# Optimization experiments

Measured on AMD Instinct MI355X. Metric: run time of the kernel, lower is better.

## Reference

```python
import jax, jax.numpy as jnp
import numpy as np

NUM_CLASSES = 3
POS_T, NEG_T = 0.5, 0.3
RATIO = 3
W_OBJ, W_CLS, W_LOC = 1.0, 1.0, 2.0


def _pairwise_iou(a, b):
    # a: [N,4] anchors, b: [G,4] gt boxes, xyxy
    ix1 = jnp.maximum(a[:, None, 0], b[None, :, 0])
    iy1 = jnp.maximum(a[:, None, 1], b[None, :, 1])
    ix2 = jnp.minimum(a[:, None, 2], b[None, :, 2])
    iy2 = jnp.minimum(a[:, None, 3], b[None, :, 3])
    inter = jnp.clip(ix2 - ix1, 0) * jnp.clip(iy2 - iy1, 0)
    area_a = (a[:, 2] - a[:, 0]) * (a[:, 3] - a[:, 1])
    area_b = (b[:, 2] - b[:, 0]) * (b[:, 3] - b[:, 1])
    union = area_a[:, None] + area_b[None, :] - inter
    return inter / jnp.maximum(union, 1e-9)


def _masked_mean(x, m):
    c = m.sum()
    return jnp.where(c > 0, (x * m).sum() / jnp.maximum(c, 1.0), 0.0)


def _per_image(pred, anc, ax, ay, aw, ah, boxes_gt, labels_gt):
    # pred: [N, 5+nc]; anc: [N,4]; boxes_gt: [G,4]; labels_gt: [G] in 1..nc
    iou = _pairwise_iou(anc, boxes_gt)              # [N, G]
    best = jnp.argmax(iou, axis=1)
    best_iou = jnp.max(iou, axis=1)
    pos = best_iou >= POS_T
    neg = best_iou < NEG_T
    mb = boxes_gt[best]                             # matched boxes [N,4]
    ml = labels_gt[best]                            # matched labels [N]
    obj_logit = pred[:, 4]
    cls_logit = pred[:, 5:]
    obj_t = pos.astype(pred.dtype)
    # BCEWithLogits (numerically stable)
    obj_loss = jnp.maximum(obj_logit, 0) - obj_logit * obj_t + jnp.log1p(jnp.exp(-jnp.abs(obj_logit)))
    # hard negative mining: top-(3*num_pos) detached obj losses among negatives
    num_pos = pos.sum()
    k = jnp.minimum(RATIO * num_pos, neg.sum())
    cand = jnp.where(neg, jax.lax.stop_gradient(obj_loss), -1.0)
    order = jnp.argsort(-cand)
    ranks = jnp.zeros_like(order).at[order].set(jnp.arange(order.shape[0], dtype=order.dtype))
    sel_neg = neg & (ranks < k)
    loss_obj = _masked_mean(obj_loss, (pos | sel_neg).astype(pred.dtype))
    # classification over positives, labels shifted to 0-based
    logp = jax.nn.log_softmax(cls_logit, axis=-1)
    tgt = jnp.clip(ml - 1, 0)
    ce = -jnp.take_along_axis(logp, tgt[:, None], axis=1)[:, 0]
    loss_cls = _masked_mean(ce, pos.astype(pred.dtype))
    # localization over positives: SmoothL1 on encoded offsets
    gx = (mb[:, 0] + mb[:, 2]) * 0.5
    gy = (mb[:, 1] + mb[:, 3]) * 0.5
    gw = jnp.maximum(mb[:, 2] - mb[:, 0], 1e-6)
    gh = jnp.maximum(mb[:, 3] - mb[:, 1], 1e-6)
    loc_tgt = jnp.stack([(gx - ax) / aw, (gy - ay) / ah,
                         jnp.log(gw / aw), jnp.log(gh / ah)], axis=1)
    d = pred[:, :4] - loc_tgt
    ad = jnp.abs(d)
    sl1 = jnp.where(ad < 1.0, 0.5 * d * d, ad - 0.5)  # [N,4]
    pm = pos.astype(pred.dtype)
    cnt = 4.0 * pm.sum()
    loss_loc = jnp.where(cnt > 0, (sl1 * pm[:, None]).sum() / jnp.maximum(cnt, 1.0), 0.0)
    return loss_obj, loss_cls, loss_loc


def _detection_loss(preds, ancs, gt_boxes, gt_labels):
    B = preds[0].shape[0]
    obj_s = 0.0
    cls_s = 0.0
    loc_s = 0.0
    for pred, anc in zip(preds, ancs):
        Bp, C, H, W = pred.shape
        p = jnp.transpose(pred, (0, 2, 3, 1)).reshape(Bp, -1, 5 + NUM_CLASSES)
        ax = (anc[:, 0] + anc[:, 2]) * 0.5
        ay = (anc[:, 1] + anc[:, 3]) * 0.5
        aw = jnp.maximum(anc[:, 2] - anc[:, 0], 1e-6)
        ah = jnp.maximum(anc[:, 3] - anc[:, 1], 1e-6)
        lo, lc, ll = jax.vmap(
            lambda pb, bb, lb: _per_image(pb, anc, ax, ay, aw, ah, bb, lb)
        )(p, gt_boxes, gt_labels)
        obj_s = obj_s + lo.sum()
        cls_s = cls_s + lc.sum()
        loc_s = loc_s + ll.sum()
    obj_m = obj_s / B
    cls_m = cls_s / B
    loc_m = loc_s / B
    total = W_OBJ * obj_m + W_CLS * cls_m + W_LOC * loc_m
    return total, obj_m, cls_m, loc_m


def setup_inputs() -> dict:
    key = jax.random.key(0)
    k = jax.random.split(key, 8)
    B, G, A = 32, 50, 3
    img = 512.0
    scales = [(128, 128), (64, 64), (32, 32)]
    C = A * (5 + NUM_CLASSES)  # 24

    def make_anchors(H, W):
        stride = img / H
        ys, xs = np.meshgrid(np.arange(H), np.arange(W), indexing="ij")
        cx = (xs + 0.5) * stride
        cy = (ys + 0.5) * stride
        per = []
        for s in (1.0, 1.5, 2.0):
            half = s * stride
            per.append(np.stack([cx - half, cy - half, cx + half, cy + half], axis=-1).reshape(-1, 4))
        b = np.stack(per, axis=1).reshape(-1, 4)  # [H*W*A, 4], A innermost
        return jnp.asarray(b, dtype=jnp.float32)

    preds = [jax.random.normal(k[i], (B, C, H, W), dtype=jnp.float32) for i, (H, W) in enumerate(scales)]
    ancs = [make_anchors(H, W) for (H, W) in scales]
    cx = jax.random.uniform(k[3], (B, G)) * 384.0 + 64.0
    cy = jax.random.uniform(k[4], (B, G)) * 384.0 + 64.0
    w = jax.random.uniform(k[5], (B, G)) * 112.0 + 16.0
    h = jax.random.uniform(k[6], (B, G)) * 112.0 + 16.0
    gt_boxes = jnp.stack([cx - w / 2, cy - h / 2, cx + w / 2, cy + h / 2], axis=-1).astype(jnp.float32)
    gt_labels = jax.random.randint(k[7], (B, G), 1, NUM_CLASSES + 1)
    return {"p0": preds[0], "p1": preds[1], "p2": preds[2],
            "a0": ancs[0], "a1": ancs[1], "a2": ancs[2],
            "gt_boxes": gt_boxes, "gt_labels": gt_labels}


def reference(p0, p1, p2, a0, a1, a2, gt_boxes, gt_labels):
    return _detection_loss([p0, p1, p2], [a0, a1, a2], gt_boxes, gt_labels)
```

## Files before the change

kernel.cpp:

```cpp
#include <hip/hip_runtime.h>

#define WS_ACC_POS   0
#define WS_ACC_NEG   96
#define WS_ACC_OBJ   192
#define WS_ACC_CLS   288
#define WS_ACC_LOC   384
#define WS_SENT      480
#define WS_H1        512
#define WS_TOTAL_U32 (512 + 96*192*2)

#define NBINS        192
#define BIN_OFF      872
#define SUM_SCALE    33554432.0f
#define INV_SUM_SCALE (1.0f/33554432.0f)

__device__ __forceinline__ float sl1f(float d){
  float ad = fabsf(d); return ad < 1.f ? 0.5f*d*d : ad - 0.5f;
}
__device__ __forceinline__ unsigned int rec_cnt(unsigned int v){
  return (v >= 0xA0000000u) ? (v - 0xAAAAAAAAu) : v;
}

__global__ __launch_bounds__(256) void k_main(
    const float* __restrict__ p0, const float* __restrict__ p1, const float* __restrict__ p2,
    const float* __restrict__ gtb, const int* __restrict__ gtl,
    unsigned int* __restrict__ ws)
{
  const int id = blockIdx.x;
  int s, bIm, chunk, H, lw; const float* p;
  if (id < 2048){ s=0; H=128; lw=7; chunk=id>>5;            bIm=id&31;          p=p0; }
  else if (id < 2560){ s=1; H=64; lw=6; chunk=(id-2048)>>5; bIm=(id-2048)&31;   p=p1; }
  else {              s=2; H=32; lw=5; chunk=(id-2560)>>5;  bIm=(id-2560)&31;   p=p2; }
  const int W = H, HW = H*W;
  const float stride = 512.0f/(float)H;
  const int g = s*32 + bIm;
  const int tid = threadIdx.x;

  __shared__ float4 sBox[52];
  __shared__ float  sArea[52], sGx[52], sGy[52], sGw[52], sGh[52];
  __shared__ int    sLbl[52];
  __shared__ int    sNk;
  __shared__ unsigned long long sH[NBINS];
  __shared__ float  sRF[3][4];
  __shared__ unsigned int sRU[2][4];

  if (tid < 64){
    const int ymin = (chunk*256)>>lw;
    const int rowc = 256>>lw;
    const float by1 = ((float)ymin+0.5f)*stride - 2.0f*stride;
    const float by2 = ((float)(ymin+rowc-1)+0.5f)*stride + 2.0f*stride;
    bool keep=false; float4 gb=make_float4(0,0,0,0); int lbl=0;
    if (tid < 50){
      gb  = *(const float4*)(gtb + ((size_t)bIm*50 + tid)*4);
      lbl = gtl[bIm*50 + tid];
      keep = (fminf(by2, gb.w) - fmaxf(by1, gb.y)) > 0.f;
    }
    unsigned long long m = __ballot(keep);
    if (keep){
      int idx = __popcll(m & ((1ull<<tid)-1ull));
      sBox[idx]=gb;
      sArea[idx]=(gb.z-gb.x)*(gb.w-gb.y);
      sGx[idx]=(gb.x+gb.z)*0.5f;  sGy[idx]=(gb.y+gb.w)*0.5f;
      sGw[idx]=fmaxf(gb.z-gb.x,1e-6f); sGh[idx]=fmaxf(gb.w-gb.y,1e-6f);
      sLbl[idx]=lbl;
    }
    if (tid==0) sNk = __popcll(m);
  }
  if (tid < NBINS) sH[tid]=0ull;
  __syncthreads();

  const int nk = sNk;
  const int hw  = chunk*256 + tid;
  const int hwW = chunk*256 + (tid & ~63);
  const int y = hw>>lw, x = hw&(W-1);
  const float cx = ((float)x+0.5f)*stride, cy = ((float)y+0.5f)*stride;

  const float* pb = p + (size_t)bIm*24*HW + hw;
  float xo[3];
  #pragma unroll
  for (int a=0;a<3;a++) xo[a] = pb[(size_t)(a*8+4)*HW];

  const int wxlo = (W >= 64) ? (hwW & (W-1)) : 0;
  const int wxhi = (W >= 64) ? (wxlo + 63)   : (W-1);
  const int wylo = hwW>>lw, wyhi = (hwW+63)>>lw;
  const float m2 = 2.0f*stride;
  const float wx1 = ((float)wxlo+0.5f)*stride - m2;
  const float wx2 = ((float)wxhi+0.5f)*stride + m2;
  const float wy1 = ((float)wylo+0.5f)*stride - m2;
  const float wy2 = ((float)wyhi+0.5f)*stride + m2;

  float half[3]; half[0]=stride; half[1]=1.5f*stride; half[2]=2.0f*stride;
  float areaA[3], bi[3], bu[3]; int bj[3];
  #pragma unroll
  for (int a=0;a<3;a++){
    const float aw = 2.0f*half[a];
    areaA[a]=aw*aw; bi[a]=0.f; bu[a]=1e-9f; bj[a]=0;
  }
  for (int j=0;j<nk;j++){
    const float4 gb = sBox[j];
    if (gb.x >= wx2 || gb.z <= wx1 || gb.y >= wy2 || gb.w <= wy1) continue;
    const float ar = sArea[j];
    #pragma unroll
    for (int a=0;a<3;a++){
      const float iy1 = fmaxf(cy-half[a], gb.y), iy2 = fminf(cy+half[a], gb.w);
      const float ih  = fmaxf(iy2-iy1, 0.f);
      const float ix1 = fmaxf(cx-half[a], gb.x), ix2 = fminf(cx+half[a], gb.z);
      const float iw  = fmaxf(ix2-ix1, 0.f);
      const float inter = iw*ih;
      const float un = areaA[a] + ar - inter;
      if (inter*bu[a] > bi[a]*un){ bi[a]=inter; bu[a]=un; bj[a]=j; }
    }
  }

  int accPos=0, accNeg=0;
  float accObj=0.f, accCls=0.f, accLoc=0.f;
  #pragma unroll
  for (int a=0;a<3;a++){
    const float bestIou = bi[a]/bu[a];
    const bool pos = bestIou >= 0.5f;
    const bool neg = bestIou < 0.3f;
    if (pos || neg){
      float objl = fmaxf(xo[a],0.f) - (pos ? xo[a] : 0.f)
                 + __logf(1.f + __expf(-fabsf(xo[a])));
      objl = fmaxf(objl, 0.f);
      if (neg){
        accNeg++;
        const int bin = min(max((int)(__float_as_uint(objl)>>20) - BIN_OFF, 0), NBINS-1);
        const unsigned long long pack =
            (1ull<<48) | (unsigned long long)__float2uint_rn(objl * SUM_SCALE);
        atomicAdd(&sH[bin], pack);
      } else {
        accPos++; accObj += objl;
        const int jb = bj[a];
        const float aw = 2.0f*half[a];
        const float c0=pb[(size_t)(a*8+5)*HW], c1=pb[(size_t)(a*8+6)*HW], c2=pb[(size_t)(a*8+7)*HW];
        const float mm = fmaxf(fmaxf(c0,c1),c2);
        const float lse = mm + __logf(__expf(c0-mm)+__expf(c1-mm)+__expf(c2-mm));
        const int t = max(sLbl[jb]-1, 0);
        const float ct = (t==0)?c0 : (t==1)?c1 : c2;
        accCls += lse - ct;
        const float tx = (sGx[jb]-cx)/aw;
        const float ty = (sGy[jb]-cy)/aw;
        const float tw = __logf(sGw[jb]/aw);
        const float th = __logf(sGh[jb]/aw);
        accLoc += sl1f(pb[(size_t)(a*8+0)*HW]-tx) + sl1f(pb[(size_t)(a*8+1)*HW]-ty)
                + sl1f(pb[(size_t)(a*8+2)*HW]-tw) + sl1f(pb[(size_t)(a*8+3)*HW]-th);
      }
    }
  }

  #pragma unroll
  for (int o=32;o;o>>=1){
    accPos += __shfl_down(accPos,o,64);
    accNeg += __shfl_down(accNeg,o,64);
    accObj += __shfl_down(accObj,o,64);
    accCls += __shfl_down(accCls,o,64);
    accLoc += __shfl_down(accLoc,o,64);
  }
  if ((tid & 63)==0){
    const int w = tid>>6;
    sRU[0][w]=(unsigned)accPos; sRU[1][w]=(unsigned)accNeg;
    sRF[0][w]=accObj; sRF[1][w]=accCls; sRF[2][w]=accLoc;
  }
  __syncthreads();
  if (tid==0){
    float* wf = (float*)ws;
    unsigned pc=0, nc=0; float ob=0,cl=0,lc=0;
    #pragma unroll
    for (int w=0;w<4;w++){ pc+=sRU[0][w]; nc+=sRU[1][w]; ob+=sRF[0][w]; cl+=sRF[1][w]; lc+=sRF[2][w]; }
    if (pc) atomicAdd(&ws[WS_ACC_POS+g], pc);
    if (nc) atomicAdd(&ws[WS_ACC_NEG+g], nc);
    if (ob!=0.f) atomicAdd(&wf[WS_ACC_OBJ+g], ob);
    if (cl!=0.f) atomicAdd(&wf[WS_ACC_CLS+g], cl);
    if (lc!=0.f) atomicAdd(&wf[WS_ACC_LOC+g], lc);
  }
  if (tid < NBINS){
    const unsigned long long v = sH[tid];
    if (v){
      unsigned long long* gH = (unsigned long long*)(ws + WS_H1) + (size_t)g*NBINS;
      atomicAdd(&gH[tid], v);
    }
  }
}

__global__ __launch_bounds__(64) void k_select(unsigned int* __restrict__ ws,
                                               float* __restrict__ out){
  const int g = blockIdx.x, lane = threadIdx.x;
  float* wf = (float*)ws;
  __shared__ int   sTie, sR;
  __shared__ float sTieAvg;

  const int pos  = (int)rec_cnt(ws[WS_ACC_POS+g]);
  const int negc = (int)rec_cnt(ws[WS_ACC_NEG+g]);
  const int k = min(3*pos, negc);
  float selSum = 0.f;

  if (k > 0){
    const unsigned long long base =
        (ws[WS_SENT]==0xAAAAAAAAu) ? 0xAAAAAAAAAAAAAAAAull : 0ull;
    const unsigned long long* gH =
        (const unsigned long long*)(ws + WS_H1) + (size_t)g*NBINS;
    unsigned int c[3]; float sm[3];
    #pragma unroll
    for (int j=0;j<3;j++){
      const unsigned long long d = gH[lane*3+j] - base;
      c[j]  = (unsigned int)(d>>48);
      sm[j] = (float)(d & 0xFFFFFFFFFFFFull) * INV_SUM_SCALE;
    }
    const unsigned int c3 = c[0]+c[1]+c[2];
    unsigned int incl = c3;
    #pragma unroll
    for (int off=1; off<64; off<<=1){
      unsigned int yv = __shfl_down(incl, off, 64);
      if (lane+off < 64) incl += yv;
    }
    const unsigned int excl = incl - c3;
    if (lane==0){ sTie = -1; sR = 0; sTieAvg = 0.f; }
    if (excl < (unsigned)k && incl >= (unsigned)k){
      unsigned int cum = excl;
      #pragma unroll
      for (int j=2;j>=0;j--){
        const unsigned int cc = c[j];
        if (cum + cc >= (unsigned)k){
          sTie = lane*3+j; sR = (int)((unsigned)k - cum);
          sTieAvg = sm[j]/(float)cc;
          break;
        }
        cum += cc;
      }
    }
    __syncthreads();
    const int tie = sTie;
    float above = 0.f;
    #pragma unroll
    for (int j=0;j<3;j++) if (lane*3+j > tie) above += sm[j];
    #pragma unroll
    for (int o=32;o;o>>=1) above += __shfl_down(above,o,64);
    selSum = above + (float)sR * sTieAvg;
  }
  if (lane==0){
    const int cObj = pos + k;
    const float lo = (cObj>0) ? (wf[WS_ACC_OBJ+g]+selSum)/(float)cObj : 0.f;
    const float lc = (pos>0)  ? wf[WS_ACC_CLS+g]/(float)pos           : 0.f;
    const float ll = (pos>0)  ? wf[WS_ACC_LOC+g]/(float)(4*pos)       : 0.f;
    const float invB = 1.f/32.f;
    atomicAdd(out+0, (lo + lc + 2.f*ll)*invB);
    atomicAdd(out+1, lo*invB);
    atomicAdd(out+2, lc*invB);
    atomicAdd(out+3, ll*invB);
  }
}

extern "C" void kernel_launch(void* const* d_in, const int* in_sizes, int n_in,
                              void* d_out, int out_size, void* d_ws, size_t ws_size,
                              hipStream_t stream){
  if (ws_size < (size_t)WS_TOTAL_U32*4) return;
  const float* p0  = (const float*)d_in[0];
  const float* p1  = (const float*)d_in[1];
  const float* p2  = (const float*)d_in[2];
  const float* gtb = (const float*)d_in[6];
  const int*   gtl = (const int*)d_in[7];
  unsigned int* ws = (unsigned int*)d_ws;
  float* out = (float*)d_out;

  hipLaunchKernelGGL(k_main,   dim3(2688), dim3(256), 0, stream, p0,p1,p2,gtb,gtl,ws);
  hipLaunchKernelGGL(k_select, dim3(96),   dim3(64),  0, stream, ws, out);
}
```

Measured before the change: 122.4 us.

## Use grid-stride persistent blocks in main kernel and pack pos/neg counters

```diff
diff --git a/kernel.cpp b/kernel.cpp
--- a/kernel.cpp
+++ b/kernel.cpp
@@ -13,6 +13,7 @@
 #define BIN_OFF      872
 #define SUM_SCALE    33554432.0f
 #define INV_SUM_SCALE (1.0f/33554432.0f)
+#define NB_MAIN      896
 
 __device__ __forceinline__ float sl1f(float d){
   float ad = fabsf(d); return ad < 1.f ? 0.5f*d*d : ad - 0.5f;
@@ -26,14 +27,6 @@
     const float* __restrict__ gtb, const int* __restrict__ gtl,
     unsigned int* __restrict__ ws)
 {
-  const int id = blockIdx.x;
-  int s, bIm, chunk, H, lw; const float* p;
-  if (id < 2048){ s=0; H=128; lw=7; chunk=id>>5;            bIm=id&31;          p=p0; }
-  else if (id < 2560){ s=1; H=64; lw=6; chunk=(id-2048)>>5; bIm=(id-2048)&31;   p=p1; }
-  else {              s=2; H=32; lw=5; chunk=(id-2560)>>5;  bIm=(id-2560)&31;   p=p2; }
-  const int W = H, HW = H*W;
-  const float stride = 512.0f/(float)H;
-  const int g = s*32 + bIm;
   const int tid = threadIdx.x;
 
   __shared__ float4 sBox[52];
@@ -42,143 +35,156 @@
   __shared__ int    sNk;
   __shared__ unsigned long long sH[NBINS];
   __shared__ float  sRF[3][4];
-  __shared__ unsigned int sRU[2][4];
-
-  if (tid < 64){
-    const int ymin = (chunk*256)>>lw;
-    const int rowc = 256>>lw;
-    const float by1 = ((float)ymin+0.5f)*stride - 2.0f*stride;
-    const float by2 = ((float)(ymin+rowc-1)+0.5f)*stride + 2.0f*stride;
-    bool keep=false; float4 gb=make_float4(0,0,0,0); int lbl=0;
-    if (tid < 50){
-      gb  = *(const float4*)(gtb + ((size_t)bIm*50 + tid)*4);
-      lbl = gtl[bIm*50 + tid];
-      keep = (fminf(by2, gb.w) - fmaxf(by1, gb.y)) > 0.f;
-    }
-    unsigned long long m = __ballot(keep);
-    if (keep){
-      int idx = __popcll(m & ((1ull<<tid)-1ull));
-      sBox[idx]=gb;
-      sArea[idx]=(gb.z-gb.x)*(gb.w-gb.y);
-      sGx[idx]=(gb.x+gb.z)*0.5f;  sGy[idx]=(gb.y+gb.w)*0.5f;
-      sGw[idx]=fmaxf(gb.z-gb.x,1e-6f); sGh[idx]=fmaxf(gb.w-gb.y,1e-6f);
-      sLbl[idx]=lbl;
-    }
-    if (tid==0) sNk = __popcll(m);
-  }
-  if (tid < NBINS) sH[tid]=0ull;
-  __syncthreads();
-
-  const int nk = sNk;
-  const int hw  = chunk*256 + tid;
-  const int hwW = chunk*256 + (tid & ~63);
-  const int y = hw>>lw, x = hw&(W-1);
-  const float cx = ((float)x+0.5f)*stride, cy = ((float)y+0.5f)*stride;
-
-  const float* pb = p + (size_t)bIm*24*HW + hw;
-  float xo[3];
-  #pragma unroll
-  for (int a=0;a<3;a++) xo[a] = pb[(size_t)(a*8+4)*HW];
-
-  const int wxlo = (W >= 64) ? (hwW & (W-1)) : 0;
-  const int wxhi = (W >= 64) ? (wxlo + 63)   : (W-1);
-  const int wylo = hwW>>lw, wyhi = (hwW+63)>>lw;
-  const float m2 = 2.0f*stride;
-  const float wx1 = ((float)wxlo+0.5f)*stride - m2;
-  const float wx2 = ((float)wxhi+0.5f)*stride + m2;
-  const float wy1 = ((float)wylo+0.5f)*stride - m2;
-  const float wy2 = ((float)wyhi+0.5f)*stride + m2;
-
-  float half[3]; half[0]=stride; half[1]=1.5f*stride; half[2]=2.0f*stride;
-  float areaA[3], bi[3], bu[3]; int bj[3];
-  #pragma unroll
-  for (int a=0;a<3;a++){
-    const float aw = 2.0f*half[a];
-    areaA[a]=aw*aw; bi[a]=0.f; bu[a]=1e-9f; bj[a]=0;
-  }
-  for (int j=0;j<nk;j++){
-    const float4 gb = sBox[j];
-    if (gb.x >= wx2 || gb.z <= wx1 || gb.y >= wy2 || gb.w <= wy1) continue;
-    const float ar = sArea[j];
+  __shared__ unsigned int sRU[4];
+
+  for (int id = blockIdx.x; id < 2688; id += NB_MAIN){
+    int s, bIm, chunk, H, lw; const float* p;
+    if (id < 2048){ s=0; H=128; lw=7; chunk=id>>5;            bIm=id&31;          p=p0; }
+    else if (id < 2560){ s=1; H=64; lw=6; chunk=(id-2048)>>5; bIm=(id-2048)&31;   p=p1; }
+    else {              s=2; H=32; lw=5; chunk=(id-2560)>>5;  bIm=(id-2560)&31;   p=p2; }
+    const int W = H, HW = H*W;
+    const float stride = 512.0f/(float)H;
+    const int g = s*32 + bIm;
+
+    const int hw  = chunk*256 + tid;
+    const int hwW = chunk*256 + (tid & ~63);
+    const int y = hw>>lw, x = hw&(W-1);
+    const float cx = ((float)x+0.5f)*stride, cy = ((float)y+0.5f)*stride;
+
+    const float* pb = p + (size_t)bIm*24*HW + hw;
+    float xo[3];
+    #pragma unroll
+    for (int a=0;a<3;a++) xo[a] = pb[(size_t)(a*8+4)*HW];
+
+    __syncthreads();
+
+    if (tid < 64){
+      const int ymin = (chunk*256)>>lw;
+      const int rowc = 256>>lw;
+      const float by1 = ((float)ymin+0.5f)*stride - 2.0f*stride;
+      const float by2 = ((float)(ymin+rowc-1)+0.5f)*stride + 2.0f*stride;
+      bool keep=false; float4 gb=make_float4(0,0,0,0); int lbl=0;
+      if (tid < 50){
+        gb  = *(const float4*)(gtb + ((size_t)bIm*50 + tid)*4);
+        lbl = gtl[bIm*50 + tid];
+        keep = (fminf(by2, gb.w) - fmaxf(by1, gb.y)) > 0.f;
+      }
+      unsigned long long m = __ballot(keep);
+      if (keep){
+        int idx = __popcll(m & ((1ull<<tid)-1ull));
+        sBox[idx]=gb;
+        sArea[idx]=(gb.z-gb.x)*(gb.w-gb.y);
+        sGx[idx]=(gb.x+gb.z)*0.5f;  sGy[idx]=(gb.y+gb.w)*0.5f;
+        sGw[idx]=fmaxf(gb.z-gb.x,1e-6f); sGh[idx]=fmaxf(gb.w-gb.y,1e-6f);
+        sLbl[idx]=lbl;
+      }
+      if (tid==0) sNk = __popcll(m);
+    }
+    if (tid < NBINS) sH[tid]=0ull;
+    __syncthreads();
+
+    const int nk = sNk;
+
+    const int wxlo = (W >= 64) ? (hwW & (W-1)) : 0;
+    const int wxhi = (W >= 64) ? (wxlo + 63)   : (W-1);
+    const int wylo = hwW>>lw, wyhi = (hwW+63)>>lw;
+    const float m2 = 2.0f*stride;
+    const float wx1 = ((float)wxlo+0.5f)*stride - m2;
+    const float wx2 = ((float)wxhi+0.5f)*stride + m2;
+    const float wy1 = ((float)wylo+0.5f)*stride - m2;
+    const float wy2 = ((float)wyhi+0.5f)*stride + m2;
+
+    float half[3]; half[0]=stride; half[1]=1.5f*stride; half[2]=2.0f*stride;
+    float areaA[3], bi[3], bu[3]; int bj[3];
     #pragma unroll
     for (int a=0;a<3;a++){
-      const float iy1 = fmaxf(cy-half[a], gb.y), iy2 = fminf(cy+half[a], gb.w);
-      const float ih  = fmaxf(iy2-iy1, 0.f);
-      const float ix1 = fmaxf(cx-half[a], gb.x), ix2 = fminf(cx+half[a], gb.z);
-      const float iw  = fmaxf(ix2-ix1, 0.f);
-      const float inter = iw*ih;
-      const float un = areaA[a] + ar - inter;
-      if (inter*bu[a] > bi[a]*un){ bi[a]=inter; bu[a]=un; bj[a]=j; }
-    }
-  }
-
-  int accPos=0, accNeg=0;
-  float accObj=0.f, accCls=0.f, accLoc=0.f;
-  #pragma unroll
-  for (int a=0;a<3;a++){
-    const float bestIou = bi[a]/bu[a];
-    const bool pos = bestIou >= 0.5f;
-    const bool neg = bestIou < 0.3f;
-    if (pos || neg){
-      float objl = fmaxf(xo[a],0.f) - (pos ? xo[a] : 0.f)
-                 + __logf(1.f + __expf(-fabsf(xo[a])));
-      objl = fmaxf(objl, 0.f);
-      if (neg){
-        accNeg++;
-        const int bin = min(max((int)(__float_as_uint(objl)>>20) - BIN_OFF, 0), NBINS-1);
-        const unsigned long long pack =
-            (1ull<<48) | (unsigned long long)__float2uint_rn(objl * SUM_SCALE);
-        atomicAdd(&sH[bin], pack);
-      } else {
-        accPos++; accObj += objl;
-        const int jb = bj[a];
-        const float aw = 2.0f*half[a];
-        const float c0=pb[(size_t)(a*8+5)*HW], c1=pb[(size_t)(a*8+6)*HW], c2=pb[(size_t)(a*8+7)*HW];
-        const float mm = fmaxf(fmaxf(c0,c1),c2);
-        const float lse = mm + __logf(__expf(c0-mm)+__expf(c1-mm)+__expf(c2-mm));
-        const int t = max(sLbl[jb]-1, 0);
-        const float ct = (t==0)?c0 : (t==1)?c1 : c2;
-        accCls += lse - ct;
-        const float tx = (sGx[jb]-cx)/aw;
-        const float ty = (sGy[jb]-cy)/aw;
-        const float tw = __logf(sGw[jb]/aw);
-        const float th = __logf(sGh[jb]/aw);
-        accLoc += sl1f(pb[(size_t)(a*8+0)*HW]-tx) + sl1f(pb[(size_t)(a*8+1)*HW]-ty)
-                + sl1f(pb[(size_t)(a*8+2)*HW]-tw) + sl1f(pb[(size_t)(a*8+3)*HW]-th);
-      }
-    }
-  }
-
-  #pragma unroll
-  for (int o=32;o;o>>=1){
-    accPos += __shfl_down(accPos,o,64);
-    accNeg += __shfl_down(accNeg,o,64);
-    accObj += __shfl_down(accObj,o,64);
-    accCls += __shfl_down(accCls,o,64);
-    accLoc += __shfl_down(accLoc,o,64);
-  }
-  if ((tid & 63)==0){
-    const int w = tid>>6;
-    sRU[0][w]=(unsigned)accPos; sRU[1][w]=(unsigned)accNeg;
-    sRF[0][w]=accObj; sRF[1][w]=accCls; sRF[2][w]=accLoc;
-  }
-  __syncthreads();
-  if (tid==0){
-    float* wf = (float*)ws;
-    unsigned pc=0, nc=0; float ob=0,cl=0,lc=0;
-    #pragma unroll
-    for (int w=0;w<4;w++){ pc+=sRU[0][w]; nc+=sRU[1][w]; ob+=sRF[0][w]; cl+=sRF[1][w]; lc+=sRF[2][w]; }
-    if (pc) atomicAdd(&ws[WS_ACC_POS+g], pc);
-    if (nc) atomicAdd(&ws[WS_ACC_NEG+g], nc);
-    if (ob!=0.f) atomicAdd(&wf[WS_ACC_OBJ+g], ob);
-    if (cl!=0.f) atomicAdd(&wf[WS_ACC_CLS+g], cl);
-    if (lc!=0.f) atomicAdd(&wf[WS_ACC_LOC+g], lc);
-  }
-  if (tid < NBINS){
-    const unsigned long long v = sH[tid];
-    if (v){
-      unsigned long long* gH = (unsigned long long*)(ws + WS_H1) + (size_t)g*NBINS;
-      atomicAdd(&gH[tid], v);
+      const float aw = 2.0f*half[a];
+      areaA[a]=aw*aw; bi[a]=0.f; bu[a]=1e-9f; bj[a]=0;
+    }
+    for (int j=0;j<nk;j++){
+      const float4 gb = sBox[j];
+      if (gb.x >= wx2 || gb.z <= wx1 || gb.y >= wy2 || gb.w <= wy1) continue;
+      const float ar = sArea[j];
+      #pragma unroll
+      for (int a=0;a<3;a++){
+        const float iy1 = fmaxf(cy-half[a], gb.y), iy2 = fminf(cy+half[a], gb.w);
+        const float ih  = fmaxf(iy2-iy1, 0.f);
+        const float ix1 = fmaxf(cx-half[a], gb.x), ix2 = fminf(cx+half[a], gb.z);
+        const float iw  = fmaxf(ix2-ix1, 0.f);
+        const float inter = iw*ih;
+        const float un = areaA[a] + ar - inter;
+        if (inter*bu[a] > bi[a]*un){ bi[a]=inter; bu[a]=un; bj[a]=j; }
+      }
+    }
+
+    int accPN=0;
+    float accObj=0.f, accCls=0.f, accLoc=0.f;
+    #pragma unroll
+    for (int a=0;a<3;a++){
+      const bool pos = bi[a] >= 0.5f*bu[a];
+      const bool neg = bi[a] < 0.3f*bu[a];
+      if (pos || neg){
+        float objl = fmaxf(xo[a],0.f) - (pos ? xo[a] : 0.f)
+                   + __logf(1.f + __expf(-fabsf(xo[a])));
+        objl = fmaxf(objl, 0.f);
+        if (neg){
+          accPN += (1<<16);
+          const int bin = min(max((int)(__float_as_uint(objl)>>20) - BIN_OFF, 0), NBINS-1);
+          const unsigned long long pack =
+              (1ull<<48) | (unsigned long long)__float2uint_rn(objl * SUM_SCALE);
+          atomicAdd(&sH[bin], pack);
+        } else {
+          accPN += 1; accObj += objl;
+          const int jb = bj[a];
+          const float aw = 2.0f*half[a];
+          const float c0=pb[(size_t)(a*8+5)*HW], c1=pb[(size_t)(a*8+6)*HW], c2=pb[(size_t)(a*8+7)*HW];
+          const float mm = fmaxf(fmaxf(c0,c1),c2);
+          const float lse = mm + __logf(__expf(c0-mm)+__expf(c1-mm)+__expf(c2-mm));
+          const int t = max(sLbl[jb]-1, 0);
+          const float ct = (t==0)?c0 : (t==1)?c1 : c2;
+          accCls += lse - ct;
+          const float tx = (sGx[jb]-cx)/aw;
+          const float ty = (sGy[jb]-cy)/aw;
+          const float tw = __logf(sGw[jb]/aw);
+          const float th = __logf(sGh[jb]/aw);
+          accLoc += sl1f(pb[(size_t)(a*8+0)*HW]-tx) + sl1f(pb[(size_t)(a*8+1)*HW]-ty)
+                  + sl1f(pb[(size_t)(a*8+2)*HW]-tw) + sl1f(pb[(size_t)(a*8+3)*HW]-th);
+        }
+      }
+    }
+
+    #pragma unroll
+    for (int o=32;o;o>>=1){
+      accPN  += __shfl_down(accPN,o,64);
+      accObj += __shfl_down(accObj,o,64);
+      accCls += __shfl_down(accCls,o,64);
+      accLoc += __shfl_down(accLoc,o,64);
+    }
+    if ((tid & 63)==0){
+      const int w = tid>>6;
+      sRU[w]=(unsigned)accPN;
+      sRF[0][w]=accObj; sRF[1][w]=accCls; sRF[2][w]=accLoc;
+    }
+    __syncthreads();
+
+    if (tid==0){
+      float* wf = (float*)ws;
+      unsigned t=0; float ob=0,cl=0,lc=0;
+      #pragma unroll
+      for (int w=0;w<4;w++){ t+=sRU[w]; ob+=sRF[0][w]; cl+=sRF[1][w]; lc+=sRF[2][w]; }
+      const unsigned pc = t & 0xFFFFu, nc = t >> 16;
+      if (pc) atomicAdd(&ws[WS_ACC_POS+g], pc);
+      if (nc) atomicAdd(&ws[WS_ACC_NEG+g], nc);
+      if (ob!=0.f) atomicAdd(&wf[WS_ACC_OBJ+g], ob);
+      if (cl!=0.f) atomicAdd(&wf[WS_ACC_CLS+g], cl);
+      if (lc!=0.f) atomicAdd(&wf[WS_ACC_LOC+g], lc);
+    }
+    if (tid < NBINS){
+      const unsigned long long v = sH[tid];
+      if (v){
+        unsigned long long* gH = (unsigned long long*)(ws + WS_H1) + (size_t)g*NBINS;
+        atomicAdd(&gH[tid], v);
+      }
     }
   }
 }
@@ -263,6 +269,6 @@
   unsigned int* ws = (unsigned int*)d_ws;
   float* out = (float*)d_out;
 
-  hipLaunchKernelGGL(k_main,   dim3(2688), dim3(256), 0, stream, p0,p1,p2,gtb,gtl,ws);
-  hipLaunchKernelGGL(k_select, dim3(96),   dim3(64),  0, stream, ws, out);
-}
+  hipLaunchKernelGGL(k_main,   dim3(NB_MAIN), dim3(256), 0, stream, p0,p1,p2,gtb,gtl,ws);
+  hipLaunchKernelGGL(k_select, dim3(96),      dim3(64),  0, stream, ws, out);
+}
```

After: 128.0 us. 4.6% more time.
